# Kernel optimization log

Measured on AMD Instinct MI355X. Metric: run time of the kernel, lower is better.

Reference implementation:

```python
import jax, jax.numpy as jnp
import numpy as np

DT = 0.001
TAU_SYN = 0.01
TAU_MEM = 0.005
THRESHOLD = 1.0
ALPHA = float(np.exp(-DT / TAU_SYN))  # syn decay
BETA = float(np.exp(-DT / TAU_MEM))   # mem decay

BATCH, IN_SIZE, OUT_SIZE = 4096, 2048, 2048


@jax.custom_vjp
def spike(x):
    # Heaviside forward with sigmoid-derivative surrogate gradient
    return (x > 0).astype(x.dtype)

def _spike_fwd(x):
    return spike(x), x

def _spike_bwd(x, g):
    s = jax.nn.sigmoid(x)
    return (g * s * (1.0 - s),)

spike.defvjp(_spike_fwd, _spike_bwd)


def setup_inputs() -> dict:
    key = jax.random.key(0)
    k1, k2, k3, k4, k5 = jax.random.split(key, 5)
    inputs = jax.random.normal(k1, (BATCH, IN_SIZE), dtype=jnp.float32)
    I = jax.random.normal(k2, (BATCH, OUT_SIZE), dtype=jnp.float32)
    V = jax.random.normal(k3, (BATCH, OUT_SIZE), dtype=jnp.float32)
    Z = jnp.zeros((BATCH, OUT_SIZE), dtype=jnp.float32)
    # initialize_weights_: ndim<=2 -> normal init
    fwd_w = jax.random.normal(k4, (IN_SIZE, OUT_SIZE), dtype=jnp.float32)
    rec_w = jax.random.normal(k5, (OUT_SIZE, OUT_SIZE), dtype=jnp.float32)
    return {"inputs": inputs, "I": I, "V": V, "Z": Z,
            "fwd_w": fwd_w, "rec_w": rec_w}


def reference(inputs, I, V, Z, fwd_w, rec_w):
    # LIFLayer.forward_Erme, single timestep
    input_current = jnp.matmul(inputs, fwd_w)          # [B, O]
    rec_current = jnp.matmul(Z, rec_w)                 # [B, O]
    is_active = 1.0 - jax.lax.stop_gradient(Z)
    next_I = ALPHA * I + input_current + rec_current
    next_V = (BETA * V + next_I) * is_active
    next_Z = spike(next_V - THRESHOLD)
    return next_Z, next_I, next_V
```

## Files before the change

### kernel.cpp

```cpp
#include <hip/hip_runtime.h>
#include <cstdint>
#include <cstddef>

typedef __bf16 bf16_t;
typedef __bf16 bf16x4 __attribute__((ext_vector_type(4)));
typedef __bf16 bf16x8 __attribute__((ext_vector_type(8)));
typedef float f32x4 __attribute__((ext_vector_type(4)));

#define M_DIM 4096
#define K_DIM 2048
#define N_DIM 2048

#define BM 128
#define BN 64
#define BK 64
#define KT (K_DIM / BK)
#define A_EL (BM * BK)
#define B_EL (BN * BK)
#define B_OFF A_EL

#define ZCAP 64

#define MFMA16(a, b, c) \
  __builtin_amdgcn_mfma_f32_16x16x32_bf16((a), (b), (c), 0, 0, 0)

__device__ __forceinline__ void gload_lds16(const bf16_t* g, bf16_t* l) {
  __builtin_amdgcn_global_load_lds(
      (const __attribute__((address_space(1))) void*)g,
      (__attribute__((address_space(3))) void*)l, 16, 0, 0);
}

__global__ __launch_bounds__(256) void convert_a(
    const float* __restrict__ inputs, bf16_t* __restrict__ abf) {
  const int g = blockIdx.x * 256 + threadIdx.x;
  const size_t base = (size_t)g * 8;
  const float4 v0 = *reinterpret_cast<const float4*>(inputs + base);
  const float4 v1 = *reinterpret_cast<const float4*>(inputs + base + 4);
  bf16x8 o;
  o[0] = (bf16_t)v0.x; o[1] = (bf16_t)v0.y;
  o[2] = (bf16_t)v0.z; o[3] = (bf16_t)v0.w;
  o[4] = (bf16_t)v1.x; o[5] = (bf16_t)v1.y;
  o[6] = (bf16_t)v1.z; o[7] = (bf16_t)v1.w;
  *reinterpret_cast<bf16x8*>(abf + base) = o;
}

__global__ __launch_bounds__(256) void transpose_w(
    const float* __restrict__ src, bf16_t* __restrict__ dst) {
  __shared__ float tile[64][65];
  const int t = threadIdx.x;
  const int k0 = blockIdx.y * 64;
  const int n0 = blockIdx.x * 64;
#pragma unroll
  for (int p = 0; p < 4; ++p) {
    const int r = p * 16 + (t >> 4);
    const int c = (t & 15) * 4;
    const float4 v = *reinterpret_cast<const float4*>(
        &src[(size_t)(k0 + r) * N_DIM + n0 + c]);
    tile[r][c + 0] = v.x;
    tile[r][c + 1] = v.y;
    tile[r][c + 2] = v.z;
    tile[r][c + 3] = v.w;
  }
  __syncthreads();
#pragma unroll
  for (int p = 0; p < 4; ++p) {
    const int n = p * 16 + (t >> 4);
    const int c = (t & 15) * 4;
    bf16x4 o;
    o[0] = (bf16_t)tile[c + 0][n];
    o[1] = (bf16_t)tile[c + 1][n];
    o[2] = (bf16_t)tile[c + 2][n];
    o[3] = (bf16_t)tile[c + 3][n];
    *reinterpret_cast<bf16x4*>(&dst[(size_t)(n0 + n) * K_DIM + k0 + c]) = o;
  }
}

__global__ __launch_bounds__(256) void scan_z(
    const float* __restrict__ Z, int* __restrict__ zcnt,
    int* __restrict__ zidx, float* __restrict__ zval) {
  const int row = blockIdx.x * 4 + (threadIdx.x >> 6);
  const int lane = threadIdx.x & 63;
  const float* zr = Z + (size_t)row * N_DIM;
  int local = 0;
#pragma unroll
  for (int c = 0; c < 32; c += 4) {
    const f32x4 v = *reinterpret_cast<const f32x4*>(zr + lane * 32 + c);
#pragma unroll
    for (int e = 0; e < 4; ++e) local += (v[e] != 0.0f) ? 1 : 0;
  }
  int pre = local;
#pragma unroll
  for (int d = 1; d < 64; d <<= 1) {
    const int up = __shfl_up(pre, d, 64);
    if (lane >= d) pre += up;
  }
  const int total = __shfl(pre, 63, 64);
  if (lane == 0) zcnt[row] = total;
  if (total > 0 && total <= ZCAP) {
    int wpos = pre - local;
    int* zi = zidx + (size_t)row * ZCAP;
    float* zv = zval + (size_t)row * ZCAP;
    for (int c = lane * 32; c < lane * 32 + 32; ++c) {
      const float v = zr[c];
      if (v != 0.0f) {
        zi[wpos] = c;
        zv[wpos] = v;
        ++wpos;
      }
    }
  }
}

__global__ __launch_bounds__(256, 2) void lif_gemm_tlp(
    const bf16_t* __restrict__ A, const bf16_t* __restrict__ W,
    const float* __restrict__ recw,
    const int* __restrict__ zcnt, const int* __restrict__ zidx,
    const float* __restrict__ zval,
    const float* __restrict__ Iin, const float* __restrict__ Vin,
    const float* __restrict__ Zin,
    float* __restrict__ outZ, float* __restrict__ outI,
    float* __restrict__ outV) {
  __shared__ __align__(16) bf16_t lds[A_EL + B_EL];

  const int tid = threadIdx.x;
  const int lane = tid & 63;
  const int wave = tid >> 6;
  const int wm = wave >> 1;
  const int wn = wave & 1;
  const int l15 = lane & 15;
  const int l4 = lane >> 4;

  const int bid = blockIdx.x;
  const int swz = (bid & 7) * 128 + (bid >> 3);
  const int m0 = (swz >> 5) * BM;
  const int n0 = (swz & 31) * BN;

  const int lr = lane >> 3;
  const int sg = (lane & 7) ^ lr;
  const bf16_t* aSrc[4];
  const bf16_t* bSrc[2];
  int aDst[4], bDst[2];
#pragma unroll
  for (int i = 0; i < 4; ++i) {
    const int r = wave * 32 + i * 8 + lr;
    aSrc[i] = A + (size_t)(m0 + r) * K_DIM + sg * 8;
    aDst[i] = r * BK + (lane & 7) * 8;
  }
#pragma unroll
  for (int i = 0; i < 2; ++i) {
    const int r = wave * 16 + i * 8 + lr;
    bSrc[i] = W + (size_t)(n0 + r) * K_DIM + sg * 8;
    bDst[i] = B_OFF + r * BK + (lane & 7) * 8;
  }

  int aBase[2], bBase[2];
#pragma unroll
  for (int ks = 0; ks < 2; ++ks) {
    const int phys = (l4 + ks * 4) ^ (l15 & 7);
    aBase[ks] = (wm * 64 + l15) * BK + phys * 8;
    bBase[ks] = B_OFF + (wn * 32 + l15) * BK + phys * 8;
  }

  f32x4 acc[4][2];
#pragma unroll
  for (int i = 0; i < 4; ++i)
#pragma unroll
    for (int j = 0; j < 2; ++j)
#pragma unroll
      for (int e = 0; e < 4; ++e) acc[i][j][e] = 0.0f;

  for (int kb = 0; kb < KT; ++kb) {
#pragma unroll
    for (int i = 0; i < 4; ++i) gload_lds16(aSrc[i], lds + aDst[i]);
#pragma unroll
    for (int i = 0; i < 2; ++i) gload_lds16(bSrc[i], lds + bDst[i]);
#pragma unroll
    for (int i = 0; i < 4; ++i) aSrc[i] += BK;
#pragma unroll
    for (int i = 0; i < 2; ++i) bSrc[i] += BK;
    __syncthreads();

    bf16x8 af[4][2], bfr[2][2];
#pragma unroll
    for (int mi = 0; mi < 4; ++mi)
#pragma unroll
      for (int ks = 0; ks < 2; ++ks)
        af[mi][ks] =
            *reinterpret_cast<const bf16x8*>(lds + aBase[ks] + mi * 1024);
#pragma unroll
    for (int ni = 0; ni < 2; ++ni)
#pragma unroll
      for (int ks = 0; ks < 2; ++ks)
        bfr[ni][ks] =
            *reinterpret_cast<const bf16x8*>(lds + bBase[ks] + ni * 1024);
#pragma unroll
    for (int mi = 0; mi < 4; ++mi)
#pragma unroll
      for (int ni = 0; ni < 2; ++ni) {
        acc[mi][ni] = MFMA16(af[mi][0], bfr[ni][0], acc[mi][ni]);
        acc[mi][ni] = MFMA16(af[mi][1], bfr[ni][1], acc[mi][ni]);
      }
    __syncthreads();
  }

  const float alpha = 0.90483741803595957f;
  const float beta = 0.81873075307798182f;
#pragma unroll
  for (int mi = 0; mi < 4; ++mi) {
#pragma unroll
    for (int j = 0; j < 4; ++j) {
      const int r = m0 + wm * 64 + mi * 16 + l4 * 4 + j;
      const int cnt = zcnt[r];
      float rec0 = 0.0f, rec1 = 0.0f;
      const int c0 = n0 + wn * 32 + l15;
      const int c1 = c0 + 16;
      if (cnt > 0) {
        if (cnt <= ZCAP) {
          const int* zi = zidx + (size_t)r * ZCAP;
          const float* zv = zval + (size_t)r * ZCAP;
          for (int s = 0; s < cnt; ++s) {
            const int o = zi[s];
            const float v = zv[s];
            rec0 += v * recw[(size_t)o * N_DIM + c0];
            rec1 += v * recw[(size_t)o * N_DIM + c1];
          }
        } else {
          const float* zr = Zin + (size_t)r * N_DIM;
          for (int o = 0; o < N_DIM; ++o) {
            const float v = zr[o];
            if (v != 0.0f) {
              rec0 += v * recw[(size_t)o * N_DIM + c0];
              rec1 += v * recw[(size_t)o * N_DIM + c1];
            }
          }
        }
      }
#pragma unroll
      for (int ni = 0; ni < 2; ++ni) {
        const int c = ni ? c1 : c0;
        const size_t idx = (size_t)r * N_DIM + c;
        const float zin = Zin[idx];
        const float rec = ni ? rec1 : rec0;
        const float nI = alpha * Iin[idx] + acc[mi][ni][j] + rec;
        const float nV = (beta * Vin[idx] + nI) * (1.0f - zin);
        outI[idx] = nI;
        outV[idx] = nV;
        outZ[idx] = (nV > 1.0f) ? 1.0f : 0.0f;
      }
    }
  }
}

extern "C" void kernel_launch(void* const* d_in, const int* in_sizes, int n_in,
                              void* d_out, int out_size, void* d_ws,
                              size_t ws_size, hipStream_t stream) {
  const float* inputs = (const float*)d_in[0];
  const float* I = (const float*)d_in[1];
  const float* V = (const float*)d_in[2];
  const float* Z = (const float*)d_in[3];
  const float* fwd_w = (const float*)d_in[4];
  const float* rec_w = (const float*)d_in[5];

  float* outZ = (float*)d_out;
  float* outI = outZ + (size_t)M_DIM * N_DIM;
  float* outV = outI + (size_t)M_DIM * N_DIM;

  bf16_t* abf = (bf16_t*)d_ws;
  bf16_t* wT = (bf16_t*)((char*)d_ws + (size_t)M_DIM * K_DIM * 2);
  char* p = (char*)d_ws + (size_t)M_DIM * K_DIM * 2 + (size_t)N_DIM * K_DIM * 2;
  int* zcnt = (int*)p;
  int* zidx = (int*)(p + M_DIM * 4);
  float* zval = (float*)(p + M_DIM * 4 + (size_t)M_DIM * ZCAP * 4);

  hipLaunchKernelGGL(convert_a, dim3((M_DIM * K_DIM) / (256 * 8)), dim3(256),
                     0, stream, inputs, abf);
  hipLaunchKernelGGL(transpose_w, dim3(N_DIM / 64, K_DIM / 64), dim3(256), 0,
                     stream, fwd_w, wT);
  hipLaunchKernelGGL(scan_z, dim3(M_DIM / 4), dim3(256), 0, stream, Z, zcnt,
                     zidx, zval);
  hipLaunchKernelGGL(lif_gemm_tlp, dim3((M_DIM / BM) * (N_DIM / BN)),
                     dim3(256), 0, stream, abf, wT, rec_w, zcnt, zidx, zval, I,
                     V, Z, outZ, outI, outV);
}
```

Measured before the change: 106.2 us.

## Double-buffer LDS with 128x128 tiles and vectorized LDS-staged epilogue

Measured after the change: 88.74 us. -16.4%, faster.

```diff
diff --git a/kernel.cpp b/kernel.cpp
--- a/kernel.cpp
+++ b/kernel.cpp
@@ -12,11 +12,12 @@
 #define N_DIM 2048
 
 #define BM 128
-#define BN 64
+#define BN 128
 #define BK 64
 #define KT (K_DIM / BK)
 #define A_EL (BM * BK)
 #define B_EL (BN * BK)
+#define PER_BUF (A_EL + B_EL)
 #define B_OFF A_EL
 
 #define ZCAP 64
@@ -111,7 +112,7 @@
   }
 }
 
-__global__ __launch_bounds__(256, 2) void lif_gemm_tlp(
+__global__ __launch_bounds__(256, 2) void lif_gemm_db(
     const bf16_t* __restrict__ A, const bf16_t* __restrict__ W,
     const float* __restrict__ recw,
     const int* __restrict__ zcnt, const int* __restrict__ zidx,
@@ -120,7 +121,7 @@
     const float* __restrict__ Zin,
     float* __restrict__ outZ, float* __restrict__ outI,
     float* __restrict__ outV) {
-  __shared__ __align__(16) bf16_t lds[A_EL + B_EL];
+  __shared__ __align__(16) bf16_t lds[2 * PER_BUF];
 
   const int tid = threadIdx.x;
   const int lane = tid & 63;
@@ -131,24 +132,20 @@
   const int l4 = lane >> 4;
 
   const int bid = blockIdx.x;
-  const int swz = (bid & 7) * 128 + (bid >> 3);
-  const int m0 = (swz >> 5) * BM;
-  const int n0 = (swz & 31) * BN;
+  const int swz = (bid & 7) * 64 + (bid >> 3);
+  const int m0 = (swz >> 4) * BM;
+  const int n0 = (swz & 15) * BN;
 
   const int lr = lane >> 3;
   const int sg = (lane & 7) ^ lr;
   const bf16_t* aSrc[4];
-  const bf16_t* bSrc[2];
-  int aDst[4], bDst[2];
+  const bf16_t* bSrc[4];
+  int aDst[4], bDst[4];
 #pragma unroll
   for (int i = 0; i < 4; ++i) {
     const int r = wave * 32 + i * 8 + lr;
     aSrc[i] = A + (size_t)(m0 + r) * K_DIM + sg * 8;
     aDst[i] = r * BK + (lane & 7) * 8;
-  }
-#pragma unroll
-  for (int i = 0; i < 2; ++i) {
-    const int r = wave * 16 + i * 8 + lr;
     bSrc[i] = W + (size_t)(n0 + r) * K_DIM + sg * 8;
     bDst[i] = B_OFF + r * BK + (lane & 7) * 8;
   }
@@ -158,95 +155,167 @@
   for (int ks = 0; ks < 2; ++ks) {
     const int phys = (l4 + ks * 4) ^ (l15 & 7);
     aBase[ks] = (wm * 64 + l15) * BK + phys * 8;
-    bBase[ks] = B_OFF + (wn * 32 + l15) * BK + phys * 8;
-  }
-
-  f32x4 acc[4][2];
+    bBase[ks] = B_OFF + (wn * 64 + l15) * BK + phys * 8;
+  }
+
+  f32x4 acc[4][4];
 #pragma unroll
   for (int i = 0; i < 4; ++i)
 #pragma unroll
-    for (int j = 0; j < 2; ++j)
+    for (int j = 0; j < 4; ++j)
 #pragma unroll
       for (int e = 0; e < 4; ++e) acc[i][j][e] = 0.0f;
 
-  for (int kb = 0; kb < KT; ++kb) {
-#pragma unroll
-    for (int i = 0; i < 4; ++i) gload_lds16(aSrc[i], lds + aDst[i]);
-#pragma unroll
-    for (int i = 0; i < 2; ++i) gload_lds16(bSrc[i], lds + bDst[i]);
-#pragma unroll
-    for (int i = 0; i < 4; ++i) aSrc[i] += BK;
-#pragma unroll
-    for (int i = 0; i < 2; ++i) bSrc[i] += BK;
-    __syncthreads();
-
-    bf16x8 af[4][2], bfr[2][2];
+#pragma unroll
+  for (int i = 0; i < 4; ++i) {
+    gload_lds16(aSrc[i], lds + aDst[i]);
+    gload_lds16(bSrc[i], lds + bDst[i]);
+  }
+#pragma unroll
+  for (int i = 0; i < 4; ++i) {
+    gload_lds16(aSrc[i] + BK, lds + PER_BUF + aDst[i]);
+    gload_lds16(bSrc[i] + BK, lds + PER_BUF + bDst[i]);
+  }
+  asm volatile("s_waitcnt vmcnt(8)" ::: "memory");
+  __builtin_amdgcn_sched_barrier(0);
+  __builtin_amdgcn_s_barrier();
+  __builtin_amdgcn_sched_barrier(0);
+
+  for (int t = 0; t < KT; ++t) {
+    const bf16_t* bufC = lds + (t & 1) * PER_BUF;
+    bf16_t* bufS = lds + (t & 1) * PER_BUF;
+
+    bf16x8 af[4][2], bfr[4][2];
 #pragma unroll
     for (int mi = 0; mi < 4; ++mi)
 #pragma unroll
       for (int ks = 0; ks < 2; ++ks)
         af[mi][ks] =
-            *reinterpret_cast<const bf16x8*>(lds + aBase[ks] + mi * 1024);
-#pragma unroll
-    for (int ni = 0; ni < 2; ++ni)
+            *reinterpret_cast<const bf16x8*>(bufC + aBase[ks] + mi * 1024);
+#pragma unroll
+    for (int ni = 0; ni < 4; ++ni)
 #pragma unroll
       for (int ks = 0; ks < 2; ++ks)
         bfr[ni][ks] =
-            *reinterpret_cast<const bf16x8*>(lds + bBase[ks] + ni * 1024);
+            *reinterpret_cast<const bf16x8*>(bufC + bBase[ks] + ni * 1024);
+    asm volatile("s_waitcnt lgkmcnt(0)" ::: "memory");
+    __builtin_amdgcn_sched_barrier(0);
+    __builtin_amdgcn_s_barrier();
+    __builtin_amdgcn_sched_barrier(0);
+
+    if (t + 2 < KT) {
+      const int kt = (t + 2) * BK;
+#pragma unroll
+      for (int i = 0; i < 4; ++i) {
+        gload_lds16(aSrc[i] + kt, bufS + aDst[i]);
+        gload_lds16(bSrc[i] + kt, bufS + bDst[i]);
+      }
+    }
+
+    __builtin_amdgcn_s_setprio(1);
 #pragma unroll
     for (int mi = 0; mi < 4; ++mi)
 #pragma unroll
-      for (int ni = 0; ni < 2; ++ni) {
+      for (int ni = 0; ni < 4; ++ni) {
         acc[mi][ni] = MFMA16(af[mi][0], bfr[ni][0], acc[mi][ni]);
         acc[mi][ni] = MFMA16(af[mi][1], bfr[ni][1], acc[mi][ni]);
       }
-    __syncthreads();
+    __builtin_amdgcn_s_setprio(0);
+    __builtin_amdgcn_sched_barrier(0);
+
+    if (t + 2 < KT) {
+      asm volatile("s_waitcnt vmcnt(8)" ::: "memory");
+    } else if (t + 1 < KT) {
+      asm volatile("s_waitcnt vmcnt(0)" ::: "memory");
+    }
+    __builtin_amdgcn_sched_barrier(0);
+    __builtin_amdgcn_s_barrier();
+    __builtin_amdgcn_sched_barrier(0);
   }
 
   const float alpha = 0.90483741803595957f;
   const float beta = 0.81873075307798182f;
+  float* swp = reinterpret_cast<float*>(lds) + wave * (16 * 66);
+  const int er = lane >> 2;
+  const int ec = (lane & 3) * 4;
+
 #pragma unroll
   for (int mi = 0; mi < 4; ++mi) {
 #pragma unroll
-    for (int j = 0; j < 4; ++j) {
-      const int r = m0 + wm * 64 + mi * 16 + l4 * 4 + j;
-      const int cnt = zcnt[r];
-      float rec0 = 0.0f, rec1 = 0.0f;
-      const int c0 = n0 + wn * 32 + l15;
-      const int c1 = c0 + 16;
-      if (cnt > 0) {
-        if (cnt <= ZCAP) {
-          const int* zi = zidx + (size_t)r * ZCAP;
-          const float* zv = zval + (size_t)r * ZCAP;
-          for (int s = 0; s < cnt; ++s) {
-            const int o = zi[s];
-            const float v = zv[s];
-            rec0 += v * recw[(size_t)o * N_DIM + c0];
-            rec1 += v * recw[(size_t)o * N_DIM + c1];
-          }
-        } else {
-          const float* zr = Zin + (size_t)r * N_DIM;
-          for (int o = 0; o < N_DIM; ++o) {
-            const float v = zr[o];
-            if (v != 0.0f) {
-              rec0 += v * recw[(size_t)o * N_DIM + c0];
-              rec1 += v * recw[(size_t)o * N_DIM + c1];
+    for (int ni = 0; ni < 4; ++ni)
+#pragma unroll
+      for (int j = 0; j < 4; ++j)
+        swp[(l4 * 4 + j) * 66 + ni * 16 + l15] = acc[mi][ni][j];
+
+    const int row = m0 + wm * 64 + mi * 16 + er;
+    const int colb = n0 + wn * 64 + ec;
+    const int cnt = zcnt[row];
+
+    f32x4 rec4[4], gate4[4];
+#pragma unroll
+    for (int cc = 0; cc < 4; ++cc)
+#pragma unroll
+      for (int e = 0; e < 4; ++e) {
+        rec4[cc][e] = 0.0f;
+        gate4[cc][e] = 1.0f;
+      }
+    if (cnt > 0) {
+      if (cnt <= ZCAP) {
+        const int* zi = zidx + (size_t)row * ZCAP;
+        const float* zv = zval + (size_t)row * ZCAP;
+        for (int s = 0; s < cnt; ++s) {
+          const int o = zi[s];
+          const float v = zv[s];
+          const float* wr = recw + (size_t)o * N_DIM + colb;
+#pragma unroll
+          for (int cc = 0; cc < 4; ++cc) {
+            const f32x4 wv = *reinterpret_cast<const f32x4*>(wr + cc * 16);
+#pragma unroll
+            for (int e = 0; e < 4; ++e) {
+              rec4[cc][e] += v * wv[e];
+              gate4[cc][e] = (o == colb + cc * 16 + e) ? (1.0f - v)
+                                                       : gate4[cc][e];
             }
           }
         }
-      }
-#pragma unroll
-      for (int ni = 0; ni < 2; ++ni) {
-        const int c = ni ? c1 : c0;
-        const size_t idx = (size_t)r * N_DIM + c;
-        const float zin = Zin[idx];
-        const float rec = ni ? rec1 : rec0;
-        const float nI = alpha * Iin[idx] + acc[mi][ni][j] + rec;
-        const float nV = (beta * Vin[idx] + nI) * (1.0f - zin);
-        outI[idx] = nI;
-        outV[idx] = nV;
-        outZ[idx] = (nV > 1.0f) ? 1.0f : 0.0f;
-      }
+      } else {
+        const float* zr = Zin + (size_t)row * N_DIM;
+        for (int o = 0; o < N_DIM; ++o) {
+          const float v = zr[o];
+          if (v != 0.0f) {
+            const float* wr = recw + (size_t)o * N_DIM + colb;
+#pragma unroll
+            for (int cc = 0; cc < 4; ++cc) {
+              const f32x4 wv = *reinterpret_cast<const f32x4*>(wr + cc * 16);
+#pragma unroll
+              for (int e = 0; e < 4; ++e) {
+                rec4[cc][e] += v * wv[e];
+                gate4[cc][e] = (o == colb + cc * 16 + e) ? (1.0f - v)
+                                                         : gate4[cc][e];
+              }
+            }
+          }
+        }
+      }
+    }
+
+    const size_t gb = (size_t)row * N_DIM + colb;
+#pragma unroll
+    for (int cc = 0; cc < 4; ++cc) {
+      const f32x4 av =
+          *reinterpret_cast<const f32x4*>(swp + er * 66 + ec + cc * 16);
+      const f32x4 iv = *reinterpret_cast<const f32x4*>(Iin + gb + cc * 16);
+      const f32x4 vv = *reinterpret_cast<const f32x4*>(Vin + gb + cc * 16);
+      f32x4 nI, nV, nZ;
+#pragma unroll
+      for (int e = 0; e < 4; ++e) {
+        nI[e] = alpha * iv[e] + av[e] + rec4[cc][e];
+        nV[e] = (beta * vv[e] + nI[e]) * gate4[cc][e];
+        nZ[e] = (nV[e] > 1.0f) ? 1.0f : 0.0f;
+      }
+      *reinterpret_cast<f32x4*>(outI + gb + cc * 16) = nI;
+      *reinterpret_cast<f32x4*>(outV + gb + cc * 16) = nV;
+      *reinterpret_cast<f32x4*>(outZ + gb + cc * 16) = nZ;
     }
   }
 }
@@ -278,7 +347,7 @@
                      stream, fwd_w, wT);
   hipLaunchKernelGGL(scan_z, dim3(M_DIM / 4), dim3(256), 0, stream, Z, zcnt,
                      zidx, zval);
-  hipLaunchKernelGGL(lif_gemm_tlp, dim3((M_DIM / BM) * (N_DIM / BN)),
+  hipLaunchKernelGGL(lif_gemm_db, dim3((M_DIM / BM) * (N_DIM / BN)),
                      dim3(256), 0, stream, abf, wT, rec_w, zcnt, zidx, zval, I,
                      V, Z, outZ, outI, outV);
 }
```
